# Kernel optimization log

Hardware: AMD Instinct MI355X
Metric: run time of the kernel (lower is better)

Reference implementation:

```python
import jax, jax.numpy as jnp
import numpy as np

N = 50000      # nodes (single 'paper' node type)
E = 800000     # edges per etype
ET = 3         # edge types
L = 3          # GAT layers (1 + num_hidden=2)
H = 4          # heads
DH = 64        # per-head dim (n_hidden // n_heads)
NH = H * DH    # 256
NC = 16        # classes
NEG_SLOPE = 0.2


def setup_inputs() -> dict:
    key = jax.random.key(0)
    ks = jax.random.split(key, 8)
    x = jax.random.normal(ks[0], (N, NH), jnp.float32)
    src = jax.random.randint(ks[1], (ET, E), 0, N, jnp.int32)
    dst = jax.random.randint(ks[2], (ET, E), 0, N, jnp.int32)
    W = jax.random.normal(ks[3], (L, ET, NH, NH), jnp.float32) * 0.05
    attn_l = jax.random.normal(ks[4], (L, ET, H, DH), jnp.float32) * 0.05
    attn_r = jax.random.normal(ks[5], (L, ET, H, DH), jnp.float32) * 0.05
    bias = jnp.zeros((L, ET, NH), jnp.float32)
    lin_w = jax.random.normal(ks[6], (NH, NC), jnp.float32) * 0.05
    lin_b = jnp.zeros((NC,), jnp.float32)
    return {"x": x, "src": src, "dst": dst, "W": W, "attn_l": attn_l,
            "attn_r": attn_r, "bias": bias, "lin_w": lin_w, "lin_b": lin_b}


def _gat(h, W_e, al, ar, b, s, d):
    # h: [N, NH] -> z: [N, H, DH]
    z = (h @ W_e).reshape(N, H, DH)
    el = jnp.sum(z * al, axis=-1)             # [N, H]  (src-side score)
    er = jnp.sum(z * ar, axis=-1)             # [N, H]  (dst-side score)
    e = jax.nn.leaky_relu(el[s] + er[d], NEG_SLOPE)   # [E, H]
    # edge softmax over incoming edges of each dst node
    m = jax.ops.segment_max(e, d, num_segments=N)     # [N, H]
    a = jnp.exp(e - m[d])                              # [E, H]
    denom = jax.ops.segment_sum(a, d, num_segments=N) # [N, H]
    alpha = a / denom[d]                               # [E, H]
    # weighted aggregation of source features
    out = jax.ops.segment_sum(alpha[:, :, None] * z[s], d, num_segments=N)  # [N, H, DH]
    return out.reshape(N, NH) + b


def reference(x, src, dst, W, attn_l, attn_r, bias, lin_w, lin_b):
    h = x
    for l in range(L):
        acc = jnp.zeros((N, NH), h.dtype)
        for t in range(ET):  # HeteroGraphConv 'sum' aggregation across etypes
            acc = acc + _gat(h, W[l, t], attn_l[l, t], attn_r[l, t],
                             bias[l, t], src[t], dst[t])
        h = acc
        if l != L - 1:
            h = jax.nn.relu(h)  # dropout is identity in eval
    return h @ lin_w + lin_b    # [N, NC]
```

## Files before the change

kernel.cpp:

```cpp
#include <hip/hip_runtime.h>
#include <hip/hip_bf16.h>
#include <math.h>

#define N_NODES 50000
#define NEDGE 800000
#define NET 3
#define LAYERS 3
#define HEADS 4
#define DHEAD 64
#define NH 256
#define NC 16
#define NEG_SLOPE 0.2f
#define MPAD 50048

typedef __attribute__((ext_vector_type(8))) short short8;
typedef __attribute__((ext_vector_type(4))) float f32x4;
typedef __attribute__((ext_vector_type(8))) _Float16 half8;

#define GLDS16(gp, lp) \
  __builtin_amdgcn_global_load_lds((const __attribute__((address_space(1))) void*)(gp), \
                                   (__attribute__((address_space(3))) void*)(lp), 16, 0, 0)

__device__ inline unsigned short f2bf(float x) {
  unsigned u = __float_as_uint(x);
  unsigned r = (u + 0x7FFFu + ((u >> 16) & 1u)) >> 16;
  return (unsigned short)r;
}
__device__ inline float bf2f(unsigned short h) { return __uint_as_float(((unsigned)h) << 16); }

__global__ void split_transpose_W(const float* __restrict__ W,
                                  unsigned short* __restrict__ WhT,
                                  unsigned short* __restrict__ WlT) {
  int i = blockIdx.x * blockDim.x + threadIdx.x;
  if (i >= LAYERS * NET * NH * NH) return;
  int mat = i >> 16, rem = i & 65535;
  int n = rem >> 8, k = rem & 255;
  float v = W[(size_t)mat * 65536 + k * 256 + n];
  unsigned short hi = f2bf(v);
  unsigned short lo = f2bf(v - bf2f(hi));
  WhT[(size_t)mat * 65536 + n * 256 + k] = hi;
  WlT[(size_t)mat * 65536 + n * 256 + k] = lo;
}

__global__ void split_kernel(const float* __restrict__ in, unsigned short* __restrict__ hi,
                             unsigned short* __restrict__ lo) {
  int i = blockIdx.x * blockDim.x + threadIdx.x;
  if (i >= N_NODES * NH / 4) return;
  float4 v = ((const float4*)in)[i];
  ushort4 h, l;
  h.x = f2bf(v.x); l.x = f2bf(v.x - bf2f(h.x));
  h.y = f2bf(v.y); l.y = f2bf(v.y - bf2f(h.y));
  h.z = f2bf(v.z); l.z = f2bf(v.z - bf2f(h.z));
  h.w = f2bf(v.w); l.w = f2bf(v.w - bf2f(h.w));
  ((ushort4*)hi)[i] = h;
  ((ushort4*)lo)[i] = l;
}

__global__ __launch_bounds__(256) void gemm_split(const unsigned short* __restrict__ Ah,
                                                  const unsigned short* __restrict__ Al,
                                                  const unsigned short* __restrict__ BhT,
                                                  const unsigned short* __restrict__ BlT,
                                                  const float* __restrict__ al,
                                                  const float* __restrict__ ar,
                                                  _Float16* __restrict__ zh,
                                                  float* __restrict__ el,
                                                  float* __restrict__ er, int M) {
  __shared__ unsigned short lds[20480];
  unsigned short* sAh = lds;
  unsigned short* sAl = lds + 2048;
  unsigned short* sBh = lds + 4096;
  unsigned short* sBl = lds + 12288;

  int tid = threadIdx.x;
  int w = tid >> 6, lane = tid & 63;
  int r16 = lane & 15, rk = lane >> 4;
  int bm = blockIdx.x * 64;

  int arow = tid >> 2, acol = (tid & 3) * 8;
  const unsigned short* pAh = Ah + (size_t)(bm + arow) * 256 + acol;
  const unsigned short* pAl = Al + (size_t)(bm + arow) * 256 + acol;

  f32x4 acc[4][4];
#pragma unroll
  for (int m = 0; m < 4; m++)
#pragma unroll
    for (int n = 0; n < 4; n++) acc[m][n] = (f32x4){0.f, 0.f, 0.f, 0.f};

  char* aldsA = (char*)lds + (size_t)w * 1024;

#pragma unroll
  for (int k0 = 0; k0 < 8; k0++) {
    GLDS16(pAh + k0 * 32, aldsA);
    GLDS16(pAl + k0 * 32, (char*)sAl + (size_t)w * 1024);
#pragma unroll
    for (int i = 0; i < 4; i++) {
      int slot = tid + i * 256;
      int nrow = slot >> 2, kcol = (slot & 3) * 8;
      size_t go = (size_t)nrow * 256 + k0 * 32 + kcol;
      char* lb = (char*)sBh + ((size_t)w * 64 + (size_t)i * 256) * 16;
      char* lb2 = (char*)sBl + ((size_t)w * 64 + (size_t)i * 256) * 16;
      GLDS16(BhT + go, lb);
      GLDS16(BlT + go, lb2);
    }
    __syncthreads();

    short8 a_h[4], a_l[4], b_h[4], b_l[4];
#pragma unroll
    for (int m = 0; m < 4; m++) {
      a_h[m] = *(const short8*)&sAh[(m * 16 + r16) * 32 + rk * 8];
      a_l[m] = *(const short8*)&sAl[(m * 16 + r16) * 32 + rk * 8];
    }
#pragma unroll
    for (int n = 0; n < 4; n++) {
      int col = w * 64 + n * 16 + r16;
      b_h[n] = *(const short8*)&sBh[col * 32 + rk * 8];
      b_l[n] = *(const short8*)&sBl[col * 32 + rk * 8];
    }
#pragma unroll
    for (int m = 0; m < 4; m++)
#pragma unroll
      for (int n = 0; n < 4; n++) {
        acc[m][n] = __builtin_amdgcn_mfma_f32_16x16x32_bf16(a_h[m], b_h[n], acc[m][n], 0, 0, 0);
        acc[m][n] = __builtin_amdgcn_mfma_f32_16x16x32_bf16(a_h[m], b_l[n], acc[m][n], 0, 0, 0);
        acc[m][n] = __builtin_amdgcn_mfma_f32_16x16x32_bf16(a_l[m], b_h[n], acc[m][n], 0, 0, 0);
      }
    __syncthreads();
  }

#pragma unroll
  for (int m = 0; m < 4; m++) {
    int row0 = bm + m * 16 + rk * 4;
#pragma unroll
    for (int n = 0; n < 4; n++) {
      int col = w * 64 + n * 16 + r16;
#pragma unroll
      for (int r = 0; r < 4; r++) {
        int row = row0 + r;
        if (row < M) zh[(size_t)row * 256 + col] = (_Float16)acc[m][n][r];
      }
    }
  }

  float alv[4], arv[4];
#pragma unroll
  for (int n = 0; n < 4; n++) {
    alv[n] = al[w * 64 + n * 16 + r16];
    arv[n] = ar[w * 64 + n * 16 + r16];
  }
#pragma unroll
  for (int m = 0; m < 4; m++) {
#pragma unroll
    for (int r = 0; r < 4; r++) {
      float pl = 0.f, pr = 0.f;
#pragma unroll
      for (int n = 0; n < 4; n++) {
        float zv = acc[m][n][r];
        pl = fmaf(zv, alv[n], pl);
        pr = fmaf(zv, arv[n], pr);
      }
      pl += __shfl_xor(pl, 1, 64); pl += __shfl_xor(pl, 2, 64);
      pl += __shfl_xor(pl, 4, 64); pl += __shfl_xor(pl, 8, 64);
      pr += __shfl_xor(pr, 1, 64); pr += __shfl_xor(pr, 2, 64);
      pr += __shfl_xor(pr, 4, 64); pr += __shfl_xor(pr, 8, 64);
      int row = bm + m * 16 + rk * 4 + r;
      if (r16 == 0 && row < M) {
        el[row * HEADS + w] = pl;
        er[row * HEADS + w] = pr;
      }
    }
  }
}

__device__ inline float leaky(float v) { return v > 0.f ? v : NEG_SLOPE * v; }

__global__ void deg_kernel(const int* __restrict__ dst, int* __restrict__ deg) {
  int e = blockIdx.x * blockDim.x + threadIdx.x;
  if (e < NEDGE) atomicAdd(&deg[dst[e]], 1);
}

__global__ __launch_bounds__(1024) void scan_kernel(const int* __restrict__ deg,
                                                    int* __restrict__ rowptr) {
  __shared__ int wsum[16];
  __shared__ int carry_s;
  int tid = threadIdx.x;
  int lane = tid & 63, wv = tid >> 6;
  if (tid == 0) { carry_s = 0; rowptr[0] = 0; }
  __syncthreads();
  for (int base = 0; base < N_NODES; base += 1024) {
    int i = base + tid;
    int v = (i < N_NODES) ? deg[i] : 0;
    int x = v;
#pragma unroll
    for (int off = 1; off < 64; off <<= 1) {
      int y = __shfl_up(x, off, 64);
      if (lane >= off) x += y;
    }
    if (lane == 63) wsum[wv] = x;
    __syncthreads();
    if (wv == 0 && lane < 16) {
      int s = wsum[lane];
#pragma unroll
      for (int off = 1; off < 16; off <<= 1) {
        int y = __shfl_up(s, off, 16);
        if (lane >= off) s += y;
      }
      wsum[lane] = s;
    }
    __syncthreads();
    int waveoff = (wv > 0) ? wsum[wv - 1] : 0;
    int incl = x + waveoff + carry_s;
    if (i < N_NODES) rowptr[i + 1] = incl;
    __syncthreads();
    if (tid == 1023) carry_s = incl;
    __syncthreads();
  }
}

__global__ void scatter_kernel(const int* __restrict__ src, const int* __restrict__ dst,
                               int* __restrict__ cursor, int* __restrict__ col, int rowoff) {
  int e = blockIdx.x * blockDim.x + threadIdx.x;
  if (e < NEDGE) {
    int d = dst[e];
    int pos = atomicAdd(&cursor[d], 1);
    col[pos] = src[e] + rowoff;
  }
}

__global__ __launch_bounds__(256) void agg3_kernel(const int* __restrict__ rowptr,
                                                   const int* __restrict__ col,
                                                   const float* __restrict__ el,
                                                   const float* __restrict__ er,
                                                   const _Float16* __restrict__ zh,
                                                   float* __restrict__ hout,
                                                   unsigned short* __restrict__ Ah,
                                                   unsigned short* __restrict__ Al,
                                                   const float* __restrict__ b0,
                                                   const float* __restrict__ b1,
                                                   const float* __restrict__ b2,
                                                   int final_layer) {
  __shared__ float s_alpha[4][128][4];
  __shared__ int s_col[4][128];

  int wv = threadIdx.x >> 6, lane = threadIdx.x & 63;
  int n = blockIdx.x * 4 + wv;
  int kk = lane & 15, hh = lane >> 4;
  int which = lane >> 5, lj = lane & 31, fh = lj >> 3;

  float v0 = 0.f, v1 = 0.f, v2 = 0.f, v3 = 0.f;
  float v4 = 0.f, v5 = 0.f, v6 = 0.f, v7 = 0.f;

  for (int t = 0; t < NET; t++) {
    int rs = rowptr[t * (N_NODES + 1) + n];
    int deg = rowptr[t * (N_NODES + 1) + n + 1] - rs;
    const int* colt = col + (size_t)t * NEDGE;
    float erh = er[((size_t)t * N_NODES + n) * HEADS + hh];

    float sm = 0.f;
    float a0 = 0.f, a1 = 0.f, a2 = 0.f, a3 = 0.f;
    float a4 = 0.f, a5 = 0.f, a6 = 0.f, a7 = 0.f;

    for (int s0 = 0; s0 < deg; s0 += 128) {
      int segN = min(128, deg - s0);
      for (int c0 = 0; c0 < segN; c0 += 16) {
        if (c0 + kk < segN) {
          int row = colt[rs + s0 + c0 + kk];
          float a = __expf(leaky(el[(size_t)row * HEADS + hh] + erh));
          sm += a;
          s_alpha[wv][c0 + kk][hh] = a;
          if (hh == 0) s_col[wv][c0 + kk] = row;
        }
      }
      int k = which;
      for (; k + 2 < segN; k += 4) {
        float aa = s_alpha[wv][k][fh];     int ra = s_col[wv][k];
        float ab = s_alpha[wv][k + 2][fh]; int rb = s_col[wv][k + 2];
        half8 va = *(const half8*)&zh[(size_t)ra * NH + lj * 8];
        half8 vb = *(const half8*)&zh[(size_t)rb * NH + lj * 8];
        a0 = fmaf(aa, (float)va[0], a0); a1 = fmaf(aa, (float)va[1], a1);
        a2 = fmaf(aa, (float)va[2], a2); a3 = fmaf(aa, (float)va[3], a3);
        a4 = fmaf(aa, (float)va[4], a4); a5 = fmaf(aa, (float)va[5], a5);
        a6 = fmaf(aa, (float)va[6], a6); a7 = fmaf(aa, (float)va[7], a7);
        a0 = fmaf(ab, (float)vb[0], a0); a1 = fmaf(ab, (float)vb[1], a1);
        a2 = fmaf(ab, (float)vb[2], a2); a3 = fmaf(ab, (float)vb[3], a3);
        a4 = fmaf(ab, (float)vb[4], a4); a5 = fmaf(ab, (float)vb[5], a5);
        a6 = fmaf(ab, (float)vb[6], a6); a7 = fmaf(ab, (float)vb[7], a7);
      }
      for (; k < segN; k += 2) {
        float aa = s_alpha[wv][k][fh];
        int ra = s_col[wv][k];
        half8 va = *(const half8*)&zh[(size_t)ra * NH + lj * 8];
        a0 = fmaf(aa, (float)va[0], a0); a1 = fmaf(aa, (float)va[1], a1);
        a2 = fmaf(aa, (float)va[2], a2); a3 = fmaf(aa, (float)va[3], a3);
        a4 = fmaf(aa, (float)va[4], a4); a5 = fmaf(aa, (float)va[5], a5);
        a6 = fmaf(aa, (float)va[6], a6); a7 = fmaf(aa, (float)va[7], a7);
      }
    }

    sm += __shfl_xor(sm, 1, 64);
    sm += __shfl_xor(sm, 2, 64);
    sm += __shfl_xor(sm, 4, 64);
    sm += __shfl_xor(sm, 8, 64);
    float inv = (deg > 0) ? 1.f / sm : 0.f;
    float invb = __shfl(inv, fh * 16, 64);

    a0 += __shfl_xor(a0, 32, 64); a1 += __shfl_xor(a1, 32, 64);
    a2 += __shfl_xor(a2, 32, 64); a3 += __shfl_xor(a3, 32, 64);
    a4 += __shfl_xor(a4, 32, 64); a5 += __shfl_xor(a5, 32, 64);
    a6 += __shfl_xor(a6, 32, 64); a7 += __shfl_xor(a7, 32, 64);

    v0 = fmaf(a0, invb, v0); v1 = fmaf(a1, invb, v1);
    v2 = fmaf(a2, invb, v2); v3 = fmaf(a3, invb, v3);
    v4 = fmaf(a4, invb, v4); v5 = fmaf(a5, invb, v5);
    v6 = fmaf(a6, invb, v6); v7 = fmaf(a7, invb, v7);
  }

  if (lane < 32) {
    int f0 = lj * 8;
    float vo[8] = {v0, v1, v2, v3, v4, v5, v6, v7};
#pragma unroll
    for (int i = 0; i < 8; i++) vo[i] += b0[f0 + i] + b1[f0 + i] + b2[f0 + i];
    if (final_layer) {
      size_t oi = (size_t)n * NH + f0;
      float4 o0 = {vo[0], vo[1], vo[2], vo[3]};
      float4 o1 = {vo[4], vo[5], vo[6], vo[7]};
      *(float4*)&hout[oi] = o0;
      *(float4*)&hout[oi + 4] = o1;
    } else {
      ushort4 hi0, hi1, lo0, lo1;
#pragma unroll
      for (int i = 0; i < 8; i++) vo[i] = fmaxf(vo[i], 0.f);
      hi0.x = f2bf(vo[0]); lo0.x = f2bf(vo[0] - bf2f(hi0.x));
      hi0.y = f2bf(vo[1]); lo0.y = f2bf(vo[1] - bf2f(hi0.y));
      hi0.z = f2bf(vo[2]); lo0.z = f2bf(vo[2] - bf2f(hi0.z));
      hi0.w = f2bf(vo[3]); lo0.w = f2bf(vo[3] - bf2f(hi0.w));
      hi1.x = f2bf(vo[4]); lo1.x = f2bf(vo[4] - bf2f(hi1.x));
      hi1.y = f2bf(vo[5]); lo1.y = f2bf(vo[5] - bf2f(hi1.y));
      hi1.z = f2bf(vo[6]); lo1.z = f2bf(vo[6] - bf2f(hi1.z));
      hi1.w = f2bf(vo[7]); lo1.w = f2bf(vo[7] - bf2f(hi1.w));
      size_t oi = (size_t)n * NH + f0;
      *(ushort4*)&Ah[oi] = hi0;
      *(ushort4*)&Ah[oi + 4] = hi1;
      *(ushort4*)&Al[oi] = lo0;
      *(ushort4*)&Al[oi + 4] = lo1;
    }
  }
}

__global__ __launch_bounds__(256) void linear_kernel(const float* __restrict__ h,
                                                     const float* __restrict__ w,
                                                     const float* __restrict__ b,
                                                     float* __restrict__ out) {
  __shared__ float part[16][17];
  int n = blockIdx.x;
  int t = threadIdx.x;
  int c = t & 15, p = t >> 4;
  float sum = 0.f;
#pragma unroll
  for (int q = 0; q < 16; q++) {
    int j = p * 16 + q;
    sum = fmaf(h[(size_t)n * NH + j], w[j * NC + c], sum);
  }
  part[p][c] = sum;
  __syncthreads();
  if (t < 16) {
    float s = 0.f;
#pragma unroll
    for (int p2 = 0; p2 < 16; p2++) s += part[p2][t];
    out[n * NC + t] = s + b[t];
  }
}

extern "C" void kernel_launch(void* const* d_in, const int* in_sizes, int n_in,
                              void* d_out, int out_size, void* d_ws, size_t ws_size,
                              hipStream_t stream) {
  const float* x      = (const float*)d_in[0];
  const int*   src    = (const int*)d_in[1];
  const int*   dst    = (const int*)d_in[2];
  const float* W      = (const float*)d_in[3];
  const float* attn_l = (const float*)d_in[4];
  const float* attn_r = (const float*)d_in[5];
  const float* bias   = (const float*)d_in[6];
  const float* lin_w  = (const float*)d_in[7];
  const float* lin_b  = (const float*)d_in[8];
  float* out = (float*)d_out;

  char* ws = (char*)d_ws;
  size_t off = 0;
  _Float16* zh = (_Float16*)(ws + off); off += (size_t)NET * N_NODES * NH * 2;
  unsigned short* Ah = (unsigned short*)(ws + off); off += (size_t)MPAD * NH * 2;
  unsigned short* Al = (unsigned short*)(ws + off); off += (size_t)MPAD * NH * 2;
  float* h = (float*)Ah;
  unsigned short* WhT = (unsigned short*)(ws + off); off += (size_t)LAYERS * NET * NH * NH * 2;
  unsigned short* WlT = (unsigned short*)(ws + off); off += (size_t)LAYERS * NET * NH * NH * 2;
  float* el = (float*)(ws + off); off += (size_t)NET * N_NODES * HEADS * 4;
  float* er = (float*)(ws + off); off += (size_t)NET * N_NODES * HEADS * 4;
  int* rowptr = (int*)(ws + off); off += (size_t)NET * (N_NODES + 1) * 4;
  int* colA   = (int*)(ws + off); off += (size_t)NET * NEDGE * 4;
  int* deg    = (int*)(ws + off); off += (size_t)N_NODES * 4;
  int* cursor = (int*)(ws + off); off += (size_t)N_NODES * 4;

  for (int t = 0; t < NET; t++) {
    const int* d_t = dst + (size_t)t * NEDGE;
    const int* s_t = src + (size_t)t * NEDGE;
    int* rp_t = rowptr + (size_t)t * (N_NODES + 1);
    hipMemsetAsync(deg, 0, (size_t)N_NODES * 4, stream);
    deg_kernel<<<(NEDGE + 255) / 256, 256, 0, stream>>>(d_t, deg);
    scan_kernel<<<1, 1024, 0, stream>>>(deg, rp_t);
    hipMemcpyAsync(cursor, rp_t, (size_t)N_NODES * 4, hipMemcpyDeviceToDevice, stream);
    scatter_kernel<<<(NEDGE + 255) / 256, 256, 0, stream>>>(s_t, d_t, cursor,
                                                            colA + (size_t)t * NEDGE,
                                                            t * N_NODES);
  }

  split_transpose_W<<<(LAYERS * NET * NH * NH + 255) / 256, 256, 0, stream>>>(W, WhT, WlT);

  split_kernel<<<(N_NODES * NH / 4 + 255) / 256, 256, 0, stream>>>(x, Ah, Al);

  for (int l = 0; l < LAYERS; l++) {
    const float* b0 = bias + (size_t)(l * NET + 0) * NH;
    const float* b1 = bias + (size_t)(l * NET + 1) * NH;
    const float* b2 = bias + (size_t)(l * NET + 2) * NH;

    for (int t = 0; t < NET; t++) {
      const unsigned short* Bh = WhT + (size_t)(l * NET + t) * NH * NH;
      const unsigned short* Bl = WlT + (size_t)(l * NET + t) * NH * NH;
      const float* al = attn_l + (size_t)(l * NET + t) * HEADS * DHEAD;
      const float* ar = attn_r + (size_t)(l * NET + t) * HEADS * DHEAD;
      gemm_split<<<MPAD / 64, 256, 0, stream>>>(Ah, Al, Bh, Bl, al, ar,
                                                zh + (size_t)t * N_NODES * NH,
                                                el + (size_t)t * N_NODES * HEADS,
                                                er + (size_t)t * N_NODES * HEADS, N_NODES);
    }
    agg3_kernel<<<N_NODES / 4, 256, 0, stream>>>(rowptr, colA, el, er, zh, h, Ah, Al,
                                                 b0, b1, b2, l == LAYERS - 1);
  }
  linear_kernel<<<N_NODES, 256, 0, stream>>>(h, lin_w, lin_b, out);
}
```

Baseline: 1.479 ms.

## Batch CSR build across edge types, merge per-etype GEMMs, deepen gather unroll

The CSR build now handles all three edge types in one pass: deg and scatter kernels take a 2D grid, and the serial single-block scan is replaced by a three-kernel multi-block scan over the concatenated degree array. The three per-etype GEMM launches per layer become one launch with blockIdx.y selecting the etype. The aggregation gather loop is unrolled to four edges per iteration so more zh loads are in flight. The aim is fewer launches, no serial 50k-element scan, and better memory-level parallelism in the gather, at the cost of more registers in agg3.

```diff
diff --git a/kernel.cpp b/kernel.cpp
--- a/kernel.cpp
+++ b/kernel.cpp
@@ -12,6 +12,8 @@
 #define NC 16
 #define NEG_SLOPE 0.2f
 #define MPAD 50048
+#define NTOT (NET * N_NODES)
+#define SCAN_BLOCKS ((NTOT + 1023) / 1024)
 
 typedef __attribute__((ext_vector_type(8))) short short8;
 typedef __attribute__((ext_vector_type(4))) float f32x4;
@@ -56,15 +58,24 @@
   ((ushort4*)lo)[i] = l;
 }
 
-__global__ __launch_bounds__(256) void gemm_split(const unsigned short* __restrict__ Ah,
-                                                  const unsigned short* __restrict__ Al,
-                                                  const unsigned short* __restrict__ BhT,
-                                                  const unsigned short* __restrict__ BlT,
-                                                  const float* __restrict__ al,
-                                                  const float* __restrict__ ar,
-                                                  _Float16* __restrict__ zh,
-                                                  float* __restrict__ el,
-                                                  float* __restrict__ er, int M) {
+__global__ __launch_bounds__(256) void gemm_split3(const unsigned short* __restrict__ Ah,
+                                                   const unsigned short* __restrict__ Al,
+                                                   const unsigned short* __restrict__ WhT_l,
+                                                   const unsigned short* __restrict__ WlT_l,
+                                                   const float* __restrict__ attn_l_l,
+                                                   const float* __restrict__ attn_r_l,
+                                                   _Float16* __restrict__ zh_all,
+                                                   float* __restrict__ el_all,
+                                                   float* __restrict__ er_all, int M) {
+  int t = blockIdx.y;
+  const unsigned short* BhT = WhT_l + (size_t)t * NH * NH;
+  const unsigned short* BlT = WlT_l + (size_t)t * NH * NH;
+  const float* al = attn_l_l + (size_t)t * NH;
+  const float* ar = attn_r_l + (size_t)t * NH;
+  _Float16* zh = zh_all + (size_t)t * N_NODES * NH;
+  float* el = el_all + (size_t)t * N_NODES * HEADS;
+  float* er = er_all + (size_t)t * N_NODES * HEADS;
+
   __shared__ unsigned short lds[20480];
   unsigned short* sAh = lds;
   unsigned short* sAl = lds + 2048;
@@ -175,55 +186,85 @@
 
 __global__ void deg_kernel(const int* __restrict__ dst, int* __restrict__ deg) {
   int e = blockIdx.x * blockDim.x + threadIdx.x;
-  if (e < NEDGE) atomicAdd(&deg[dst[e]], 1);
-}
-
-__global__ __launch_bounds__(1024) void scan_kernel(const int* __restrict__ deg,
-                                                    int* __restrict__ rowptr) {
+  int t = blockIdx.y;
+  atomicAdd(&deg[t * N_NODES + dst[(size_t)t * NEDGE + e]], 1);
+}
+
+__global__ __launch_bounds__(1024) void scan1_kernel(const int* __restrict__ deg,
+                                                     int* __restrict__ incl,
+                                                     int* __restrict__ bsum) {
   __shared__ int wsum[16];
-  __shared__ int carry_s;
+  int tid = threadIdx.x;
+  int gid = blockIdx.x * 1024 + tid;
+  int lane = tid & 63, wv = tid >> 6;
+  int v = (gid < NTOT) ? deg[gid] : 0;
+  int x = v;
+#pragma unroll
+  for (int off = 1; off < 64; off <<= 1) {
+    int y = __shfl_up(x, off, 64);
+    if (lane >= off) x += y;
+  }
+  if (lane == 63) wsum[wv] = x;
+  __syncthreads();
+  if (wv == 0 && lane < 16) {
+    int s = wsum[lane];
+#pragma unroll
+    for (int off = 1; off < 16; off <<= 1) {
+      int y = __shfl_up(s, off, 16);
+      if (lane >= off) s += y;
+    }
+    wsum[lane] = s;
+  }
+  __syncthreads();
+  int waveoff = (wv > 0) ? wsum[wv - 1] : 0;
+  int inclv = x + waveoff;
+  if (gid < NTOT) incl[gid] = inclv;
+  if (tid == 1023) bsum[blockIdx.x] = inclv;
+}
+
+__global__ __launch_bounds__(256) void scan2_kernel(int* __restrict__ bsum, int nb) {
+  __shared__ int wsum[4];
   int tid = threadIdx.x;
   int lane = tid & 63, wv = tid >> 6;
-  if (tid == 0) { carry_s = 0; rowptr[0] = 0; }
+  int v = (tid < nb) ? bsum[tid] : 0;
+  int x = v;
+#pragma unroll
+  for (int off = 1; off < 64; off <<= 1) {
+    int y = __shfl_up(x, off, 64);
+    if (lane >= off) x += y;
+  }
+  if (lane == 63) wsum[wv] = x;
   __syncthreads();
-  for (int base = 0; base < N_NODES; base += 1024) {
-    int i = base + tid;
-    int v = (i < N_NODES) ? deg[i] : 0;
-    int x = v;
-#pragma unroll
-    for (int off = 1; off < 64; off <<= 1) {
-      int y = __shfl_up(x, off, 64);
-      if (lane >= off) x += y;
-    }
-    if (lane == 63) wsum[wv] = x;
-    __syncthreads();
-    if (wv == 0 && lane < 16) {
-      int s = wsum[lane];
-#pragma unroll
-      for (int off = 1; off < 16; off <<= 1) {
-        int y = __shfl_up(s, off, 16);
-        if (lane >= off) s += y;
-      }
-      wsum[lane] = s;
-    }
-    __syncthreads();
-    int waveoff = (wv > 0) ? wsum[wv - 1] : 0;
-    int incl = x + waveoff + carry_s;
-    if (i < N_NODES) rowptr[i + 1] = incl;
-    __syncthreads();
-    if (tid == 1023) carry_s = incl;
-    __syncthreads();
-  }
+  if (wv == 0 && lane < 4) {
+    int s = wsum[lane];
+#pragma unroll
+    for (int off = 1; off < 4; off <<= 1) {
+      int y = __shfl_up(s, off, 4);
+      if (lane >= off) s += y;
+    }
+    wsum[lane] = s;
+  }
+  __syncthreads();
+  int waveoff = (wv > 0) ? wsum[wv - 1] : 0;
+  if (tid < nb) bsum[tid] = x + waveoff - v;
+}
+
+__global__ __launch_bounds__(1024) void scan3_kernel(const int* __restrict__ incl,
+                                                     const int* __restrict__ bsum,
+                                                     int* __restrict__ rowptr) {
+  int tid = threadIdx.x;
+  int gid = blockIdx.x * 1024 + tid;
+  if (gid < NTOT) rowptr[gid + 1] = incl[gid] + bsum[blockIdx.x];
+  if (gid == 0) rowptr[0] = 0;
 }
 
 __global__ void scatter_kernel(const int* __restrict__ src, const int* __restrict__ dst,
-                               int* __restrict__ cursor, int* __restrict__ col, int rowoff) {
+                               int* __restrict__ cursor, int* __restrict__ col) {
   int e = blockIdx.x * blockDim.x + threadIdx.x;
-  if (e < NEDGE) {
-    int d = dst[e];
-    int pos = atomicAdd(&cursor[d], 1);
-    col[pos] = src[e] + rowoff;
-  }
+  int t = blockIdx.y;
+  int d = dst[(size_t)t * NEDGE + e];
+  int pos = atomicAdd(&cursor[t * N_NODES + d], 1);
+  col[pos] = src[(size_t)t * NEDGE + e] + t * N_NODES;
 }
 
 __global__ __launch_bounds__(256) void agg3_kernel(const int* __restrict__ rowptr,
@@ -250,10 +291,10 @@
   float v4 = 0.f, v5 = 0.f, v6 = 0.f, v7 = 0.f;
 
   for (int t = 0; t < NET; t++) {
-    int rs = rowptr[t * (N_NODES + 1) + n];
-    int deg = rowptr[t * (N_NODES + 1) + n + 1] - rs;
-    const int* colt = col + (size_t)t * NEDGE;
-    float erh = er[((size_t)t * N_NODES + n) * HEADS + hh];
+    int gn = t * N_NODES + n;
+    int rs = rowptr[gn];
+    int deg = rowptr[gn + 1] - rs;
+    float erh = er[(size_t)gn * HEADS + hh];
 
     float sm = 0.f;
     float a0 = 0.f, a1 = 0.f, a2 = 0.f, a3 = 0.f;
@@ -263,7 +304,7 @@
       int segN = min(128, deg - s0);
       for (int c0 = 0; c0 < segN; c0 += 16) {
         if (c0 + kk < segN) {
-          int row = colt[rs + s0 + c0 + kk];
+          int row = col[rs + s0 + c0 + kk];
           float a = __expf(leaky(el[(size_t)row * HEADS + hh] + erh));
           sm += a;
           s_alpha[wv][c0 + kk][hh] = a;
@@ -271,11 +312,15 @@
         }
       }
       int k = which;
-      for (; k + 2 < segN; k += 4) {
+      for (; k + 6 < segN; k += 8) {
         float aa = s_alpha[wv][k][fh];     int ra = s_col[wv][k];
         float ab = s_alpha[wv][k + 2][fh]; int rb = s_col[wv][k + 2];
+        float ac = s_alpha[wv][k + 4][fh]; int rc = s_col[wv][k + 4];
+        float ad = s_alpha[wv][k + 6][fh]; int rd = s_col[wv][k + 6];
         half8 va = *(const half8*)&zh[(size_t)ra * NH + lj * 8];
         half8 vb = *(const half8*)&zh[(size_t)rb * NH + lj * 8];
+        half8 vc = *(const half8*)&zh[(size_t)rc * NH + lj * 8];
+        half8 vd = *(const half8*)&zh[(size_t)rd * NH + lj * 8];
         a0 = fmaf(aa, (float)va[0], a0); a1 = fmaf(aa, (float)va[1], a1);
         a2 = fmaf(aa, (float)va[2], a2); a3 = fmaf(aa, (float)va[3], a3);
         a4 = fmaf(aa, (float)va[4], a4); a5 = fmaf(aa, (float)va[5], a5);
@@ -284,6 +329,14 @@
         a2 = fmaf(ab, (float)vb[2], a2); a3 = fmaf(ab, (float)vb[3], a3);
         a4 = fmaf(ab, (float)vb[4], a4); a5 = fmaf(ab, (float)vb[5], a5);
         a6 = fmaf(ab, (float)vb[6], a6); a7 = fmaf(ab, (float)vb[7], a7);
+        a0 = fmaf(ac, (float)vc[0], a0); a1 = fmaf(ac, (float)vc[1], a1);
+        a2 = fmaf(ac, (float)vc[2], a2); a3 = fmaf(ac, (float)vc[3], a3);
+        a4 = fmaf(ac, (float)vc[4], a4); a5 = fmaf(ac, (float)vc[5], a5);
+        a6 = fmaf(ac, (float)vc[6], a6); a7 = fmaf(ac, (float)vc[7], a7);
+        a0 = fmaf(ad, (float)vd[0], a0); a1 = fmaf(ad, (float)vd[1], a1);
+        a2 = fmaf(ad, (float)vd[2], a2); a3 = fmaf(ad, (float)vd[3], a3);
+        a4 = fmaf(ad, (float)vd[4], a4); a5 = fmaf(ad, (float)vd[5], a5);
+        a6 = fmaf(ad, (float)vd[6], a6); a7 = fmaf(ad, (float)vd[7], a7);
       }
       for (; k < segN; k += 2) {
         float aa = s_alpha[wv][k][fh];
@@ -392,25 +445,22 @@
   float* h = (float*)Ah;
   unsigned short* WhT = (unsigned short*)(ws + off); off += (size_t)LAYERS * NET * NH * NH * 2;
   unsigned short* WlT = (unsigned short*)(ws + off); off += (size_t)LAYERS * NET * NH * NH * 2;
-  float* el = (float*)(ws + off); off += (size_t)NET * N_NODES * HEADS * 4;
-  float* er = (float*)(ws + off); off += (size_t)NET * N_NODES * HEADS * 4;
-  int* rowptr = (int*)(ws + off); off += (size_t)NET * (N_NODES + 1) * 4;
+  float* el = (float*)(ws + off); off += (size_t)NTOT * HEADS * 4;
+  float* er = (float*)(ws + off); off += (size_t)NTOT * HEADS * 4;
+  int* rowptr = (int*)(ws + off); off += (size_t)(NTOT + 1) * 4;
   int* colA   = (int*)(ws + off); off += (size_t)NET * NEDGE * 4;
-  int* deg    = (int*)(ws + off); off += (size_t)N_NODES * 4;
-  int* cursor = (int*)(ws + off); off += (size_t)N_NODES * 4;
-
-  for (int t = 0; t < NET; t++) {
-    const int* d_t = dst + (size_t)t * NEDGE;
-    const int* s_t = src + (size_t)t * NEDGE;
-    int* rp_t = rowptr + (size_t)t * (N_NODES + 1);
-    hipMemsetAsync(deg, 0, (size_t)N_NODES * 4, stream);
-    deg_kernel<<<(NEDGE + 255) / 256, 256, 0, stream>>>(d_t, deg);
-    scan_kernel<<<1, 1024, 0, stream>>>(deg, rp_t);
-    hipMemcpyAsync(cursor, rp_t, (size_t)N_NODES * 4, hipMemcpyDeviceToDevice, stream);
-    scatter_kernel<<<(NEDGE + 255) / 256, 256, 0, stream>>>(s_t, d_t, cursor,
-                                                            colA + (size_t)t * NEDGE,
-                                                            t * N_NODES);
-  }
+  int* deg    = (int*)(ws + off); off += (size_t)NTOT * 4;
+  int* cursor = (int*)(ws + off); off += (size_t)NTOT * 4;
+  int* incl   = (int*)(ws + off); off += (size_t)NTOT * 4;
+  int* bsum   = (int*)(ws + off); off += 256 * 4;
+
+  hipMemsetAsync(deg, 0, (size_t)NTOT * 4, stream);
+  deg_kernel<<<dim3(NEDGE / 256, NET), 256, 0, stream>>>(dst, deg);
+  scan1_kernel<<<SCAN_BLOCKS, 1024, 0, stream>>>(deg, incl, bsum);
+  scan2_kernel<<<1, 256, 0, stream>>>(bsum, SCAN_BLOCKS);
+  scan3_kernel<<<SCAN_BLOCKS, 1024, 0, stream>>>(incl, bsum, rowptr);
+  hipMemcpyAsync(cursor, rowptr, (size_t)NTOT * 4, hipMemcpyDeviceToDevice, stream);
+  scatter_kernel<<<dim3(NEDGE / 256, NET), 256, 0, stream>>>(src, dst, cursor, colA);
 
   split_transpose_W<<<(LAYERS * NET * NH * NH + 255) / 256, 256, 0, stream>>>(W, WhT, WlT);
 
@@ -421,16 +471,12 @@
     const float* b1 = bias + (size_t)(l * NET + 1) * NH;
     const float* b2 = bias + (size_t)(l * NET + 2) * NH;
 
-    for (int t = 0; t < NET; t++) {
-      const unsigned short* Bh = WhT + (size_t)(l * NET + t) * NH * NH;
-      const unsigned short* Bl = WlT + (size_t)(l * NET + t) * NH * NH;
-      const float* al = attn_l + (size_t)(l * NET + t) * HEADS * DHEAD;
-      const float* ar = attn_r + (size_t)(l * NET + t) * HEADS * DHEAD;
-      gemm_split<<<MPAD / 64, 256, 0, stream>>>(Ah, Al, Bh, Bl, al, ar,
-                                                zh + (size_t)t * N_NODES * NH,
-                                                el + (size_t)t * N_NODES * HEADS,
-                                                er + (size_t)t * N_NODES * HEADS, N_NODES);
-    }
+    gemm_split3<<<dim3(MPAD / 64, NET), 256, 0, stream>>>(
+        Ah, Al,
+        WhT + (size_t)l * NET * NH * NH, WlT + (size_t)l * NET * NH * NH,
+        attn_l + (size_t)l * NET * NH, attn_r + (size_t)l * NET * NH,
+        zh, el, er, N_NODES);
+
     agg3_kernel<<<N_NODES / 4, 256, 0, stream>>>(rowptr, colA, el, er, zh, h, Ah, Al,
                                                  b0, b1, b2, l == LAYERS - 1);
   }
```

Result: faster. 1.315 ms (-11.1%).
